# Optimization experiments

Hardware: AMD Instinct MI355X
Metric: run time of the kernel (lower is better)

The kernel has to match this reference:

```python
import jax, jax.numpy as jnp
import numpy as np

Q_DIM = 1024
K_DIM = 1024
V_DIM = 1024
ATTEN_DIM = 1024
NUM_HEADS = 16
HEAD_DIM = ATTEN_DIM // NUM_HEADS
B, L = 4, 2048


def setup_inputs() -> dict:
    key = jax.random.key(0)
    ks = jax.random.split(key, 11)
    s = 0.02
    return {
        "query": jax.random.normal(ks[0], (B, L, Q_DIM), dtype=jnp.float32),
        "key":   jax.random.normal(ks[1], (B, L, K_DIM), dtype=jnp.float32),
        "value": jax.random.normal(ks[2], (B, L, V_DIM), dtype=jnp.float32),
        "Wq": jax.random.normal(ks[3], (Q_DIM, ATTEN_DIM), dtype=jnp.float32) * s,
        "bq": jnp.zeros((ATTEN_DIM,), dtype=jnp.float32),
        "Wk": jax.random.normal(ks[4], (K_DIM, ATTEN_DIM), dtype=jnp.float32) * s,
        "bk": jnp.zeros((ATTEN_DIM,), dtype=jnp.float32),
        "Wv": jax.random.normal(ks[5], (V_DIM, ATTEN_DIM), dtype=jnp.float32) * s,
        "bv": jnp.zeros((ATTEN_DIM,), dtype=jnp.float32),
        "Wo": jax.random.normal(ks[6], (ATTEN_DIM, V_DIM), dtype=jnp.float32) * s,
        "bo": jnp.zeros((V_DIM,), dtype=jnp.float32),
    }


def reference(query, key, value, Wq, bq, Wk, bk, Wv, bv, Wo, bo):
    # QKV projections
    q = query @ Wq + bq        # [B, L, A]
    k = key   @ Wk + bk        # [B, L, A]
    v = value @ Wv + bv        # [B, L, A]
    # split heads: [B, L, H, D]
    def split_heads(x):
        return x.reshape(x.shape[:-1] + (NUM_HEADS, HEAD_DIM))
    q, k, v = split_heads(q), split_heads(k), split_heads(v)
    scale = 1.0 / (HEAD_DIM ** 0.5)
    # scores: [B, H, Lq, Lk]
    scores = jnp.einsum("bqhd,bkhd->bhqk", q, k) * scale
    attn = jax.nn.softmax(scores, axis=-1)
    out = jnp.einsum("bhqk,bkhd->bqhd", attn, v)  # [B, Lq, H, D]
    out = out.reshape(out.shape[0], out.shape[1], ATTEN_DIM)
    return out @ Wo + bo
```

## Files before the change

### kernel.cpp

```cpp
#include <hip/hip_runtime.h>
#include <stdint.h>

#define L_SEQ 2048
#define BATCH 4
#define ADIM  1024
#define NH    16
#define HD    64
#define KT    128

typedef __attribute__((ext_vector_type(8))) short bf16x8;
typedef __attribute__((ext_vector_type(4))) float f32x4;

__device__ __forceinline__ short f2bf(float f) {
    union { float f; unsigned u; } x; x.f = f;
    unsigned r = x.u + 0x7fffu + ((x.u >> 16) & 1u);
    return (short)(r >> 16);
}

__device__ __forceinline__ void async_ld16(void* lds, const void* g) {
    __builtin_amdgcn_global_load_lds(
        (const __attribute__((address_space(1))) void*)g,
        (__attribute__((address_space(3))) void*)lds, 16, 0, 0);
}

__global__ void cvt3_kernel(const float* __restrict__ s0, const float* __restrict__ s1,
                            const float* __restrict__ s2, short* __restrict__ dst, int n4) {
    int i = blockIdx.x * blockDim.x + threadIdx.x;
    if (i >= n4) return;
    int z = blockIdx.y;
    const float* src = (z == 0) ? s0 : (z == 1) ? s1 : s2;
    float4 v = reinterpret_cast<const float4*>(src)[i];
    short4 s;
    s.x = f2bf(v.x); s.y = f2bf(v.y); s.z = f2bf(v.z); s.w = f2bf(v.w);
    reinterpret_cast<short4*>(dst + (size_t)z * (BATCH * L_SEQ * ADIM))[i] = s;
}

__global__ void transpose4_kernel(const float* __restrict__ W0, const float* __restrict__ W1,
                                  const float* __restrict__ W2, const float* __restrict__ W3,
                                  short* __restrict__ outb) {
    __shared__ float t[32][33];
    int z = blockIdx.z;
    const float* in = (z == 0) ? W0 : (z == 1) ? W1 : (z == 2) ? W2 : W3;
    short* out = outb + (size_t)z * (ADIM * ADIM);
    int x  = blockIdx.x * 32 + threadIdx.x;
    int y0 = blockIdx.y * 32 + threadIdx.y;
#pragma unroll
    for (int j = 0; j < 4; ++j)
        t[threadIdx.y + 8 * j][threadIdx.x] = in[(y0 + 8 * j) * 1024 + x];
    __syncthreads();
    int x2 = blockIdx.y * 32 + threadIdx.x;
    int y2 = blockIdx.x * 32 + threadIdx.y;
#pragma unroll
    for (int j = 0; j < 4; ++j)
        out[(y2 + 8 * j) * 1024 + x2] = f2bf(t[threadIdx.x][threadIdx.y + 8 * j]);
}

__device__ __forceinline__ void gemm_core(const short* __restrict__ A,
                                          const short* __restrict__ BT,
                                          const float* __restrict__ bias,
                                          void* __restrict__ Cout,
                                          int mode, float scalemul) {
    const int K = 1024, N = 1024;
    __shared__ __align__(16) short smem[8192];
    short* As = smem;
    short* Bs = smem + 4096;
    int tid = threadIdx.x;
    int wave = tid >> 6, lane = tid & 63, quad = lane >> 4, l16 = lane & 15;
    int wm = wave & 1, wn = wave >> 1;
    int m0 = blockIdx.y * 128, n0 = blockIdx.x * 128;
    f32x4 acc[4][4] = {};

    int row = tid >> 2, ck = tid & 3;
    const short* gA0 = A  + (size_t)(m0 + row) * K + ck * 8;
    const short* gA1 = gA0 + (size_t)64 * K;
    const short* gB0 = BT + (size_t)(n0 + row) * K + ck * 8;
    const short* gB1 = gB0 + (size_t)64 * K;
    short* lA0 = As + tid * 8;  short* lA1 = As + tid * 8 + 2048;
    short* lB0 = Bs + tid * 8;  short* lB1 = Bs + tid * 8 + 2048;

    for (int kb = 0; kb < K; kb += 32) {
        async_ld16(lA0, gA0); async_ld16(lA1, gA1);
        async_ld16(lB0, gB0); async_ld16(lB1, gB1);
        gA0 += 32; gA1 += 32; gB0 += 32; gB1 += 32;
        __syncthreads();
        bf16x8 af[4], bf[4];
#pragma unroll
        for (int mt = 0; mt < 4; ++mt)
            af[mt] = *(const bf16x8*)&As[(wm * 64 + mt * 16 + l16) * 32 + quad * 8];
#pragma unroll
        for (int nt = 0; nt < 4; ++nt)
            bf[nt] = *(const bf16x8*)&Bs[(wn * 64 + nt * 16 + l16) * 32 + quad * 8];
#pragma unroll
        for (int mt = 0; mt < 4; ++mt)
#pragma unroll
            for (int nt = 0; nt < 4; ++nt)
                acc[mt][nt] = __builtin_amdgcn_mfma_f32_16x16x32_bf16(
                    af[mt], bf[nt], acc[mt][nt], 0, 0, 0);
        __syncthreads();
    }

    if (mode == 0) {
#pragma unroll
        for (int nt = 0; nt < 4; ++nt) {
            int col = n0 + wn * 64 + nt * 16 + l16;
            float bv = bias[col];
#pragma unroll
            for (int mt = 0; mt < 4; ++mt)
#pragma unroll
                for (int r = 0; r < 4; ++r) {
                    int rw = m0 + wm * 64 + mt * 16 + quad * 4 + r;
                    ((short*)Cout)[(size_t)rw * N + col] = f2bf((acc[mt][nt][r] + bv) * scalemul);
                }
        }
    } else if (mode == 1) {
        short* tsc = smem + wave * 1152;
        int cr = lane >> 2, sg = lane & 3;
#pragma unroll
        for (int nt = 0; nt < 4; ++nt) {
            int col = n0 + wn * 64 + nt * 16 + l16;
            float bv = bias[col];
#pragma unroll
            for (int mt = 0; mt < 4; ++mt) {
                short4 p;
                p.x = f2bf(acc[mt][nt][0] + bv);
                p.y = f2bf(acc[mt][nt][1] + bv);
                p.z = f2bf(acc[mt][nt][2] + bv);
                p.w = f2bf(acc[mt][nt][3] + bv);
                *(short4*)&tsc[l16 * 72 + mt * 16 + quad * 4] = p;
            }
            bf16x8 v0 = *(const bf16x8*)&tsc[cr * 72 + sg * 16];
            bf16x8 v1 = *(const bf16x8*)&tsc[cr * 72 + sg * 16 + 8];
            int colg = n0 + wn * 64 + nt * 16 + cr;
            int hh = colg >> 6, dd = colg & 63;
            int rwb = m0 + wm * 64 + sg * 16;
            int bb = rwb >> 11, lk = rwb & 2047;
            short* dst = (short*)Cout + (((size_t)bb * NH + hh) * HD + dd) * L_SEQ + lk;
            *(bf16x8*)dst = v0;
            *(bf16x8*)(dst + 8) = v1;
        }
    } else {
#pragma unroll
        for (int nt = 0; nt < 4; ++nt) {
            int col = n0 + wn * 64 + nt * 16 + l16;
            float bv = bias[col];
#pragma unroll
            for (int mt = 0; mt < 4; ++mt)
#pragma unroll
                for (int r = 0; r < 4; ++r) {
                    int rw = m0 + wm * 64 + mt * 16 + quad * 4 + r;
                    ((float*)Cout)[(size_t)rw * N + col] = acc[mt][nt][r] + bv;
                }
        }
    }
}

__global__ __launch_bounds__(256)
void gemm_one(const short* __restrict__ A, const short* __restrict__ BT,
              const float* __restrict__ bias, void* __restrict__ Cout,
              int mode, float scalemul) {
    gemm_core(A, BT, bias, Cout, mode, scalemul);
}

__global__ __launch_bounds__(256)
void qkv_gemm(const short* __restrict__ Xbase, const short* __restrict__ WTbase,
              const float* __restrict__ bq, const float* __restrict__ bk,
              const float* __restrict__ bv,
              short* __restrict__ Qb, short* __restrict__ Kb, short* __restrict__ VTout,
              float qscale) {
    int z = blockIdx.z;
    const short* A  = Xbase + (size_t)z * (BATCH * L_SEQ * ADIM);
    const short* BT = WTbase + (size_t)z * (ADIM * ADIM);
    const float* bias = (z == 0) ? bq : (z == 1) ? bk : bv;
    void* out = (z == 0) ? (void*)Qb : (z == 1) ? (void*)Kb : (void*)VTout;
    int mode = (z == 2) ? 1 : 0;
    float sm = (z == 0) ? qscale : 1.0f;
    gemm_core(A, BT, bias, out, mode, sm);
}

#define KS_OFF 0
#define VS_OFF (KT * 72)
#define PS_OFF (VS_OFF + 64 * 136)
#define LDS_TOT (PS_OFF + 4 * 16 * 136)

__global__ __launch_bounds__(256, 3)
void attn_kernel(const short* __restrict__ Qb, const short* __restrict__ Kb,
                 const short* __restrict__ VT, short* __restrict__ Oout) {
    __shared__ __align__(16) short lds[LDS_TOT];
    int tid = threadIdx.x;
    int wave = tid >> 6, lane = tid & 63, quad = lane >> 4, l16 = lane & 15;
    int h = blockIdx.y, b = blockIdx.z;
    int q0 = blockIdx.x * 128 + wave * 32;

    int qrowA = b * L_SEQ + q0 + l16;
    const short* qpA = Qb + (size_t)qrowA * ADIM + h * HD;
    bf16x8 qloA = *(const bf16x8*)&qpA[quad * 8];
    bf16x8 qhiA = *(const bf16x8*)&qpA[32 + quad * 8];
    const short* qpB = qpA + (size_t)16 * ADIM;
    bf16x8 qloB = *(const bf16x8*)&qpB[quad * 8];
    bf16x8 qhiB = *(const bf16x8*)&qpB[32 + quad * 8];

    const short* Kbase = Kb + (size_t)b * L_SEQ * ADIM + h * HD;
    const short* Vbase = VT + ((size_t)(b * NH + h) * HD) * L_SEQ;
    const short* gp[9];
    int lof[9], gst[9];
#pragma unroll
    for (int s = 0; s < 9; ++s) {
        int idx = tid + s * 256;
        if (idx < 1152) {
            int row = idx / 9, ck = idx - row * 9;
            gp[s] = Kbase + (size_t)row * ADIM + ck * 8;
            lof[s] = KS_OFF + idx * 8;
            gst[s] = KT * ADIM;
        } else {
            int j = idx - 1152; if (j >= 1088) j = 0;
            int row = j / 17, ck = j - row * 17;
            gp[s] = Vbase + (size_t)row * L_SEQ + ck * 8;
            lof[s] = VS_OFF + j * 8;
            gst[s] = KT;
        }
    }

    f32x4 lpA = {}, lpB = {};
    f32x4 oA[4] = {}, oB[4] = {};
    short* psw = lds + PS_OFF + wave * 16 * 136;

    for (int kb = 0; kb < L_SEQ; kb += KT) {
        __syncthreads();
#pragma unroll
        for (int s = 0; s < 8; ++s) {
            async_ld16(lds + lof[s], gp[s]);
            gp[s] += gst[s];
        }
        if (tid < 192) async_ld16(lds + lof[8], gp[8]);
        gp[8] += gst[8];
        __syncthreads();

        f32x4 sA[8], sB[8];
#pragma unroll
        for (int nt = 0; nt < 8; ++nt) {
            const short* kr = lds + KS_OFF + (nt * 16 + l16) * 72;
            bf16x8 k0 = *(const bf16x8*)&kr[quad * 8];
            bf16x8 k1 = *(const bf16x8*)&kr[32 + quad * 8];
            f32x4 zA = {}, zB = {};
            zA = __builtin_amdgcn_mfma_f32_16x16x32_bf16(qloA, k0, zA, 0, 0, 0);
            zB = __builtin_amdgcn_mfma_f32_16x16x32_bf16(qloB, k0, zB, 0, 0, 0);
            zA = __builtin_amdgcn_mfma_f32_16x16x32_bf16(qhiA, k1, zA, 0, 0, 0);
            zB = __builtin_amdgcn_mfma_f32_16x16x32_bf16(qhiB, k1, zB, 0, 0, 0);
            sA[nt] = zA; sB[nt] = zB;
        }

#pragma unroll
        for (int nt = 0; nt < 8; ++nt)
#pragma unroll
            for (int r = 0; r < 4; ++r) {
                float pA = __builtin_amdgcn_exp2f(sA[nt][r]);
                float pB = __builtin_amdgcn_exp2f(sB[nt][r]);
                sA[nt][r] = pA; sB[nt][r] = pB;
                lpA[r] += pA; lpB[r] += pB;
            }

#pragma unroll
        for (int nt = 0; nt < 8; nt += 2)
#pragma unroll
            for (int r = 0; r < 4; ++r) {
                int a = (quad * 4 + r) * 136 + nt * 16 + l16;
#if __has_builtin(__builtin_amdgcn_cvt_pk_bf16_f32)
                auto pk = __builtin_amdgcn_cvt_pk_bf16_f32(sA[nt][r], sA[nt + 1][r]);
                unsigned u; __builtin_memcpy(&u, &pk, 4);
                psw[a]      = (short)(u & 0xffffu);
                psw[a + 16] = (short)(u >> 16);
#else
                psw[a]      = f2bf(sA[nt][r]);
                psw[a + 16] = f2bf(sA[nt + 1][r]);
#endif
            }
        bf16x8 pfA[4];
#pragma unroll
        for (int c = 0; c < 4; ++c)
            pfA[c] = *(const bf16x8*)&psw[l16 * 136 + c * 32 + quad * 8];

#pragma unroll
        for (int nt = 0; nt < 8; nt += 2)
#pragma unroll
            for (int r = 0; r < 4; ++r) {
                int a = (quad * 4 + r) * 136 + nt * 16 + l16;
#if __has_builtin(__builtin_amdgcn_cvt_pk_bf16_f32)
                auto pk = __builtin_amdgcn_cvt_pk_bf16_f32(sB[nt][r], sB[nt + 1][r]);
                unsigned u; __builtin_memcpy(&u, &pk, 4);
                psw[a]      = (short)(u & 0xffffu);
                psw[a + 16] = (short)(u >> 16);
#else
                psw[a]      = f2bf(sB[nt][r]);
                psw[a + 16] = f2bf(sB[nt + 1][r]);
#endif
            }
        bf16x8 pfB[4];
#pragma unroll
        for (int c = 0; c < 4; ++c)
            pfB[c] = *(const bf16x8*)&psw[l16 * 136 + c * 32 + quad * 8];

#pragma unroll
        for (int nt = 0; nt < 4; ++nt) {
            const short* vr = lds + VS_OFF + (nt * 16 + l16) * 136;
#pragma unroll
            for (int c = 0; c < 4; ++c) {
                bf16x8 vf = *(const bf16x8*)&vr[c * 32 + quad * 8];
                oA[nt] = __builtin_amdgcn_mfma_f32_16x16x32_bf16(pfA[c], vf, oA[nt], 0, 0, 0);
                oB[nt] = __builtin_amdgcn_mfma_f32_16x16x32_bf16(pfB[c], vf, oB[nt], 0, 0, 0);
            }
        }
    }

#pragma unroll
    for (int r = 0; r < 4; ++r) {
        float vA = lpA[r], vB = lpB[r];
        vA += __shfl_xor(vA, 1); vB += __shfl_xor(vB, 1);
        vA += __shfl_xor(vA, 2); vB += __shfl_xor(vB, 2);
        vA += __shfl_xor(vA, 4); vB += __shfl_xor(vB, 4);
        vA += __shfl_xor(vA, 8); vB += __shfl_xor(vB, 8);
        float invA = __builtin_amdgcn_rcpf(vA);
        float invB = __builtin_amdgcn_rcpf(vB);
        int rowA = b * L_SEQ + q0 + quad * 4 + r;
#pragma unroll
        for (int nt = 0; nt < 4; ++nt) {
            int col = h * HD + nt * 16 + l16;
            Oout[(size_t)rowA * ADIM + col] = f2bf(oA[nt][r] * invA);
            Oout[(size_t)(rowA + 16) * ADIM + col] = f2bf(oB[nt][r] * invB);
        }
    }
}

extern "C" void kernel_launch(void* const* d_in, const int* in_sizes, int n_in,
                              void* d_out, int out_size, void* d_ws, size_t ws_size,
                              hipStream_t stream) {
    const float* query = (const float*)d_in[0];
    const float* keyp  = (const float*)d_in[1];
    const float* value = (const float*)d_in[2];
    const float* Wq = (const float*)d_in[3];
    const float* bq = (const float*)d_in[4];
    const float* Wk = (const float*)d_in[5];
    const float* bk = (const float*)d_in[6];
    const float* Wv = (const float*)d_in[7];
    const float* bv = (const float*)d_in[8];
    const float* Wo = (const float*)d_in[9];
    const float* bo = (const float*)d_in[10];

    const float QSCALE = 0.125f * 1.44269504f;
    const size_t MB = 1ull << 20;
    const int n4 = (BATCH * L_SEQ * ADIM) / 4;
    char* w = (char*)d_ws;
    dim3 tblk(32, 8);
    dim3 gemm_grid(ADIM / 128, (BATCH * L_SEQ) / 128);
    dim3 attn_grid(L_SEQ / 128, NH, BATCH);

    if (ws_size >= 104 * MB) {
        short* X0  = (short*)(w);
        short* WT  = (short*)(w + 48 * MB);
        short* VT  = (short*)(w + 56 * MB);
        short* Kb  = (short*)(w + 72 * MB);
        short* Qb  = (short*)(w + 88 * MB);
        short* AO  = X0;

        cvt3_kernel<<<dim3(n4 / 256, 3), 256, 0, stream>>>(query, keyp, value, X0, n4);
        transpose4_kernel<<<dim3(32, 32, 4), tblk, 0, stream>>>(Wq, Wk, Wv, Wo, WT);
        qkv_gemm<<<dim3(ADIM / 128, (BATCH * L_SEQ) / 128, 3), 256, 0, stream>>>(
            X0, WT, bq, bk, bv, Qb, Kb, VT, QSCALE);
        attn_kernel<<<attn_grid, 256, 0, stream>>>(Qb, Kb, VT, AO);
        gemm_one<<<gemm_grid, 256, 0, stream>>>(AO, WT + (size_t)3 * ADIM * ADIM, bo,
                                                d_out, 2, 1.0f);
    } else {
        short* X0  = (short*)(w);
        short* WT  = (short*)(w + 16 * MB);
        short* VT  = (short*)(w + 24 * MB);
        short* Kb  = (short*)(w + 40 * MB);
        short* Qb  = (short*)(w + 56 * MB);

        transpose4_kernel<<<dim3(32, 32, 4), tblk, 0, stream>>>(Wq, Wk, Wv, Wo, WT);
        cvt3_kernel<<<dim3(n4 / 256, 1), 256, 0, stream>>>(query, query, query, X0, n4);
        gemm_one<<<gemm_grid, 256, 0, stream>>>(X0, WT, bq, Qb, 0, QSCALE);
        cvt3_kernel<<<dim3(n4 / 256, 1), 256, 0, stream>>>(keyp, keyp, keyp, X0, n4);
        gemm_one<<<gemm_grid, 256, 0, stream>>>(X0, WT + (size_t)ADIM * ADIM, bk, Kb, 0, 1.0f);
        cvt3_kernel<<<dim3(n4 / 256, 1), 256, 0, stream>>>(value, value, value, X0, n4);
        gemm_one<<<gemm_grid, 256, 0, stream>>>(X0, WT + (size_t)2 * ADIM * ADIM, bv, VT, 1, 1.0f);
        attn_kernel<<<attn_grid, 256, 0, stream>>>(Qb, Kb, VT, X0);
        gemm_one<<<gemm_grid, 256, 0, stream>>>(X0, WT + (size_t)3 * ADIM * ADIM, bo,
                                                d_out, 2, 1.0f);
    }
}
```

Baseline: 405.1 us.

## Shrink attention tiles, XOR-swizzle LDS, and remap blocks for locality

Attention now uses 64-query blocks of 128 threads and 64-key tiles instead of 128/256 threads and 128-key tiles. LDS padding is replaced by an XOR swizzle on the K, V and P buffers, and a 1D grid is remapped so that consecutive blocks group by (batch, head) slots, which should improve L2 reuse of K/V. This raises occupancy and cuts LDS footprint, but it doubles the number of barrier-separated loop iterations and the total K/V reloads per query row.

Result: slower. 431.3 us (+6.5%).

```diff
diff --git a/kernel.cpp b/kernel.cpp
--- a/kernel.cpp
+++ b/kernel.cpp
@@ -6,7 +6,7 @@
 #define ADIM  1024
 #define NH    16
 #define HD    64
-#define KT    128
+#define KT    64
 
 typedef __attribute__((ext_vector_type(8))) short bf16x8;
 typedef __attribute__((ext_vector_type(4))) float f32x4;
@@ -177,22 +177,26 @@
     gemm_core(A, BT, bias, out, mode, sm);
 }
 
-#define KS_OFF 0
-#define VS_OFF (KT * 72)
-#define PS_OFF (VS_OFF + 64 * 136)
-#define LDS_TOT (PS_OFF + 4 * 16 * 136)
-
-__global__ __launch_bounds__(256, 3)
+#define VS_OFF 4096
+#define PS_OFF 8192
+#define LDS_TOT (PS_OFF + 2 * 16 * 64)
+
+__global__ __launch_bounds__(128, 4)
 void attn_kernel(const short* __restrict__ Qb, const short* __restrict__ Kb,
                  const short* __restrict__ VT, short* __restrict__ Oout) {
     __shared__ __align__(16) short lds[LDS_TOT];
     int tid = threadIdx.x;
     int wave = tid >> 6, lane = tid & 63, quad = lane >> 4, l16 = lane & 15;
-    int h = blockIdx.y, b = blockIdx.z;
-    int q0 = blockIdx.x * 128 + wave * 32;
-
-    int qrowA = b * L_SEQ + q0 + l16;
-    const short* qpA = Qb + (size_t)qrowA * ADIM + h * HD;
+    int x7 = l16 & 7;
+
+    int id = blockIdx.x;
+    int slot = id & 7, within = id >> 3;
+    int bh = slot * 8 + (within & 7);
+    int qt = within >> 3;
+    int b = bh >> 4, h = bh & 15;
+    int q0 = qt * 64 + wave * 32;
+
+    const short* qpA = Qb + (size_t)(b * L_SEQ + q0 + l16) * ADIM + h * HD;
     bf16x8 qloA = *(const bf16x8*)&qpA[quad * 8];
     bf16x8 qhiA = *(const bf16x8*)&qpA[32 + quad * 8];
     const short* qpB = qpA + (size_t)16 * ADIM;
@@ -201,46 +205,44 @@
 
     const short* Kbase = Kb + (size_t)b * L_SEQ * ADIM + h * HD;
     const short* Vbase = VT + ((size_t)(b * NH + h) * HD) * L_SEQ;
-    const short* gp[9];
-    int lof[9], gst[9];
-#pragma unroll
-    for (int s = 0; s < 9; ++s) {
-        int idx = tid + s * 256;
-        if (idx < 1152) {
-            int row = idx / 9, ck = idx - row * 9;
-            gp[s] = Kbase + (size_t)row * ADIM + ck * 8;
-            lof[s] = KS_OFF + idx * 8;
-            gst[s] = KT * ADIM;
+    const short* gp[8];
+    int lof[8], gstp[8];
+#pragma unroll
+    for (int s = 0; s < 8; ++s) {
+        int idx = tid + s * 128;
+        if (idx < 512) {
+            int row = idx >> 3, cs = idx & 7, cl = cs ^ (row & 7);
+            gp[s] = Kbase + (size_t)row * ADIM + cl * 8;
+            lof[s] = idx * 8;
+            gstp[s] = KT * ADIM;
         } else {
-            int j = idx - 1152; if (j >= 1088) j = 0;
-            int row = j / 17, ck = j - row * 17;
-            gp[s] = Vbase + (size_t)row * L_SEQ + ck * 8;
+            int j = idx - 512;
+            int row = j >> 3, cs = j & 7, cl = cs ^ (row & 7);
+            gp[s] = Vbase + (size_t)row * L_SEQ + cl * 8;
             lof[s] = VS_OFF + j * 8;
-            gst[s] = KT;
+            gstp[s] = KT;
         }
     }
 
     f32x4 lpA = {}, lpB = {};
     f32x4 oA[4] = {}, oB[4] = {};
-    short* psw = lds + PS_OFF + wave * 16 * 136;
+    short* psw = lds + PS_OFF + wave * 1024;
 
     for (int kb = 0; kb < L_SEQ; kb += KT) {
         __syncthreads();
 #pragma unroll
         for (int s = 0; s < 8; ++s) {
             async_ld16(lds + lof[s], gp[s]);
-            gp[s] += gst[s];
-        }
-        if (tid < 192) async_ld16(lds + lof[8], gp[8]);
-        gp[8] += gst[8];
+            gp[s] += gstp[s];
+        }
         __syncthreads();
 
-        f32x4 sA[8], sB[8];
-#pragma unroll
-        for (int nt = 0; nt < 8; ++nt) {
-            const short* kr = lds + KS_OFF + (nt * 16 + l16) * 72;
-            bf16x8 k0 = *(const bf16x8*)&kr[quad * 8];
-            bf16x8 k1 = *(const bf16x8*)&kr[32 + quad * 8];
+        f32x4 sA[4], sB[4];
+#pragma unroll
+        for (int nt = 0; nt < 4; ++nt) {
+            const short* kr = lds + (nt * 16 + l16) * 64;
+            bf16x8 k0 = *(const bf16x8*)&kr[(quad ^ x7) * 8];
+            bf16x8 k1 = *(const bf16x8*)&kr[((quad + 4) ^ x7) * 8];
             f32x4 zA = {}, zB = {};
             zA = __builtin_amdgcn_mfma_f32_16x16x32_bf16(qloA, k0, zA, 0, 0, 0);
             zB = __builtin_amdgcn_mfma_f32_16x16x32_bf16(qloB, k0, zB, 0, 0, 0);
@@ -250,7 +252,7 @@
         }
 
 #pragma unroll
-        for (int nt = 0; nt < 8; ++nt)
+        for (int nt = 0; nt < 4; ++nt)
 #pragma unroll
             for (int r = 0; r < 4; ++r) {
                 float pA = __builtin_amdgcn_exp2f(sA[nt][r]);
@@ -260,51 +262,61 @@
             }
 
 #pragma unroll
-        for (int nt = 0; nt < 8; nt += 2)
+        for (int np = 0; np < 2; ++np) {
+            int nt = np * 2;
 #pragma unroll
             for (int r = 0; r < 4; ++r) {
-                int a = (quad * 4 + r) * 136 + nt * 16 + l16;
+                int qr = quad * 4 + r;
+                int base = qr * 64 + x7;
+                int csA = (nt * 2 + (l16 >> 3)) ^ (qr & 7);
+                int csB = ((nt + 1) * 2 + (l16 >> 3)) ^ (qr & 7);
 #if __has_builtin(__builtin_amdgcn_cvt_pk_bf16_f32)
                 auto pk = __builtin_amdgcn_cvt_pk_bf16_f32(sA[nt][r], sA[nt + 1][r]);
                 unsigned u; __builtin_memcpy(&u, &pk, 4);
-                psw[a]      = (short)(u & 0xffffu);
-                psw[a + 16] = (short)(u >> 16);
+                psw[base + csA * 8] = (short)(u & 0xffffu);
+                psw[base + csB * 8] = (short)(u >> 16);
 #else
-                psw[a]      = f2bf(sA[nt][r]);
-                psw[a + 16] = f2bf(sA[nt + 1][r]);
+                psw[base + csA * 8] = f2bf(sA[nt][r]);
+                psw[base + csB * 8] = f2bf(sA[nt + 1][r]);
 #endif
             }
-        bf16x8 pfA[4];
-#pragma unroll
-        for (int c = 0; c < 4; ++c)
-            pfA[c] = *(const bf16x8*)&psw[l16 * 136 + c * 32 + quad * 8];
-
-#pragma unroll
-        for (int nt = 0; nt < 8; nt += 2)
+        }
+        bf16x8 pfA[2];
+#pragma unroll
+        for (int c = 0; c < 2; ++c)
+            pfA[c] = *(const bf16x8*)&psw[l16 * 64 + ((c * 4 + quad) ^ x7) * 8];
+
+#pragma unroll
+        for (int np = 0; np < 2; ++np) {
+            int nt = np * 2;
 #pragma unroll
             for (int r = 0; r < 4; ++r) {
-                int a = (quad * 4 + r) * 136 + nt * 16 + l16;
+                int qr = quad * 4 + r;
+                int base = qr * 64 + x7;
+                int csA = (nt * 2 + (l16 >> 3)) ^ (qr & 7);
+                int csB = ((nt + 1) * 2 + (l16 >> 3)) ^ (qr & 7);
 #if __has_builtin(__builtin_amdgcn_cvt_pk_bf16_f32)
                 auto pk = __builtin_amdgcn_cvt_pk_bf16_f32(sB[nt][r], sB[nt + 1][r]);
                 unsigned u; __builtin_memcpy(&u, &pk, 4);
-                psw[a]      = (short)(u & 0xffffu);
-                psw[a + 16] = (short)(u >> 16);
+                psw[base + csA * 8] = (short)(u & 0xffffu);
+                psw[base + csB * 8] = (short)(u >> 16);
 #else
-                psw[a]      = f2bf(sB[nt][r]);
-                psw[a + 16] = f2bf(sB[nt + 1][r]);
+                psw[base + csA * 8] = f2bf(sB[nt][r]);
+                psw[base + csB * 8] = f2bf(sB[nt + 1][r]);
 #endif
             }
-        bf16x8 pfB[4];
-#pragma unroll
-        for (int c = 0; c < 4; ++c)
-            pfB[c] = *(const bf16x8*)&psw[l16 * 136 + c * 32 + quad * 8];
-
-#pragma unroll
-        for (int nt = 0; nt < 4; ++nt) {
-            const short* vr = lds + VS_OFF + (nt * 16 + l16) * 136;
-#pragma unroll
-            for (int c = 0; c < 4; ++c) {
-                bf16x8 vf = *(const bf16x8*)&vr[c * 32 + quad * 8];
+        }
+        bf16x8 pfB[2];
+#pragma unroll
+        for (int c = 0; c < 2; ++c)
+            pfB[c] = *(const bf16x8*)&psw[l16 * 64 + ((c * 4 + quad) ^ x7) * 8];
+
+#pragma unroll
+        for (int nt = 0; nt < 4; ++nt) {
+            const short* vr = lds + VS_OFF + (nt * 16 + l16) * 64;
+#pragma unroll
+            for (int c = 0; c < 2; ++c) {
+                bf16x8 vf = *(const bf16x8*)&vr[((c * 4 + quad) ^ x7) * 8];
                 oA[nt] = __builtin_amdgcn_mfma_f32_16x16x32_bf16(pfA[c], vf, oA[nt], 0, 0, 0);
                 oB[nt] = __builtin_amdgcn_mfma_f32_16x16x32_bf16(pfB[c], vf, oB[nt], 0, 0, 0);
             }
@@ -351,7 +363,7 @@
     char* w = (char*)d_ws;
     dim3 tblk(32, 8);
     dim3 gemm_grid(ADIM / 128, (BATCH * L_SEQ) / 128);
-    dim3 attn_grid(L_SEQ / 128, NH, BATCH);
+    const int attn_blocks = (BATCH * NH * L_SEQ) / 64;
 
     if (ws_size >= 104 * MB) {
         short* X0  = (short*)(w);
@@ -365,7 +377,7 @@
         transpose4_kernel<<<dim3(32, 32, 4), tblk, 0, stream>>>(Wq, Wk, Wv, Wo, WT);
         qkv_gemm<<<dim3(ADIM / 128, (BATCH * L_SEQ) / 128, 3), 256, 0, stream>>>(
             X0, WT, bq, bk, bv, Qb, Kb, VT, QSCALE);
-        attn_kernel<<<attn_grid, 256, 0, stream>>>(Qb, Kb, VT, AO);
+        attn_kernel<<<attn_blocks, 128, 0, stream>>>(Qb, Kb, VT, AO);
         gemm_one<<<gemm_grid, 256, 0, stream>>>(AO, WT + (size_t)3 * ADIM * ADIM, bo,
                                                 d_out, 2, 1.0f);
     } else {
@@ -382,7 +394,7 @@
         gemm_one<<<gemm_grid, 256, 0, stream>>>(X0, WT + (size_t)ADIM * ADIM, bk, Kb, 0, 1.0f);
         cvt3_kernel<<<dim3(n4 / 256, 1), 256, 0, stream>>>(value, value, value, X0, n4);
         gemm_one<<<gemm_grid, 256, 0, stream>>>(X0, WT + (size_t)2 * ADIM * ADIM, bv, VT, 1, 1.0f);
-        attn_kernel<<<attn_grid, 256, 0, stream>>>(Qb, Kb, VT, X0);
+        attn_kernel<<<attn_blocks, 128, 0, stream>>>(Qb, Kb, VT, X0);
         gemm_one<<<gemm_grid, 256, 0, stream>>>(X0, WT + (size_t)3 * ADIM * ADIM, bo,
                                                 d_out, 2, 1.0f);
     }
```
